# Kernel tuning notes

Hardware: AMD Instinct MI355X
Metric: run time of the kernel (lower is better)

The kernel has to match this reference:

```python
import jax, jax.numpy as jnp
import numpy as np

L, B, C, S = 4, 256, 512, 64   # layers, batch, channels, spatial (8x8 pooled map)
N = 50000                      # training-bank size per layer
K = 20                         # neighbors for LID


def setup_inputs() -> dict:
    key = jax.random.key(0)
    k1, k2 = jax.random.split(key)
    feats = jax.random.normal(k1, (L, B, C, S), dtype=jnp.float32)
    bank = jax.random.normal(k2, (L, N, C), dtype=jnp.float32)
    return {"feats": feats, "bank": bank, "k": K}


def reference(feats, bank, k):
    # per-layer spatial mean pool: f.view(B, C, -1).mean(dim=2)
    q = feats.mean(axis=-1)                                   # [L, B, C]
    # pairwise Euclidean distances query-vs-bank per layer
    q2 = jnp.sum(q * q, axis=-1)                              # [L, B]
    b2 = jnp.sum(bank * bank, axis=-1)                        # [L, N]
    cross = jnp.einsum('lbc,lnc->lbn', q, bank)               # [L, B, N]
    d2 = q2[:, :, None] + b2[:, None, :] - 2.0 * cross
    dist = jnp.sqrt(jnp.maximum(d2, 0.0))                     # [L, B, N]
    # k+1 smallest distances, ascending (sklearn kneighbors), drop nearest
    neg_top, _ = jax.lax.top_k(-dist, k + 1)                  # [L, B, k+1]
    dk = -neg_top[..., 1:]                                    # [L, B, k] ascending
    r_k = dk[..., -1:]                                        # k-th NN distance
    logs = jnp.log(dk / r_k)                                  # [L, B, k]
    lids = -(k / jnp.sum(logs, axis=-1))                      # [L, B]
    return jnp.transpose(lids, (1, 0))                        # [B, L]
```

## Files before the change

### kernel.cpp

```cpp
#include <hip/hip_runtime.h>
#include <hip/hip_bf16.h>

#define L_ 4
#define B_ 256
#define C_ 512
#define N_ 50000
#define K_ 20
#define NLIST 21
#define NCH 128
#define BIGF 3.0e38f
#define BN 64
#define KS 32
#define NKS 16
#define NT_ 7

#define BS0_O 0u
#define BS1_O 4096u
#define B2V_O 8192u
#define SD_O  8448u
#define SMEM_BYTES 45056

typedef __attribute__((ext_vector_type(8))) short short8;
typedef __attribute__((ext_vector_type(4))) float f32x4;

__device__ __forceinline__ unsigned pk2(float lo, float hi) {
    __hip_bfloat162 h = __float22bfloat162_rn(make_float2(lo, hi));
    return *reinterpret_cast<unsigned*>(&h);
}
__device__ __forceinline__ float sq4(float4 v) {
    return v.x*v.x + v.y*v.y + v.z*v.z + v.w*v.w;
}

#define LGKM_BAR() do { asm volatile("s_waitcnt lgkmcnt(0)" ::: "memory"); \
                        __builtin_amdgcn_s_barrier(); } while (0)

__global__ void qmean_kernel(const float* __restrict__ feats,
                             unsigned short* __restrict__ qbf)
{
    int gtid = blockIdx.x * 256 + threadIdx.x;
    int wid  = gtid >> 6;
    int lane = threadIdx.x & 63;
    const float4* src = reinterpret_cast<const float4*>(feats) + (size_t)wid * 64 + lane;
    float4 v = *src;
    float s = v.x + v.y + v.z + v.w;
    s += __shfl_xor(s, 1); s += __shfl_xor(s, 2);
    s += __shfl_xor(s, 4); s += __shfl_xor(s, 8);
    if ((lane & 15) == 0) {
        const int flat = wid * 4 + (lane >> 4);
        const int c    = flat & (C_ - 1);
        const int rowg = flat >> 9;
        const int l    = rowg >> 8;
        const int b    = rowg & (B_ - 1);
        const int kb = c >> 5, rh = (c >> 3) & 3, e = c & 7;
        const int band = b >> 5, m = (b >> 4) & 1, cl = b & 15;
        const size_t idx =
            ((size_t)(((l*16 + kb)*8 + band)*2 + m)*4 + rh)*128 + cl*8 + e;
        __hip_bfloat16 h = __float2bfloat16(s * (1.0f / 64.0f));
        qbf[idx] = *reinterpret_cast<unsigned short*>(&h);
    }
}

__global__ __launch_bounds__(512, 4)
void dist_topk_kernel(const float* __restrict__ bank,
                      const unsigned short* __restrict__ qbf,
                      float* __restrict__ lists)
{
    __shared__ __align__(16) unsigned char smem[SMEM_BYTES];
    float* b2v = reinterpret_cast<float*>(smem + B2V_O);
    float* sd  = reinterpret_cast<float*>(smem + SD_O);
    float* mg  = reinterpret_cast<float*>(smem);

    const int tid = threadIdx.x;
    const int l   = blockIdx.x >> 7;
    const int nc  = blockIdx.x & 127;

    const float* bb = bank + (size_t)l * N_ * C_;
    const int n0   = (nc * 3125) >> 3;
    const int n1   = ((nc + 1) * 3125) >> 3;
    const int n1m1 = n1 - 1;

    const int lane = tid & 63;
    const int wv   = tid >> 6;
    const int c_lo = lane & 15;
    const int r_hi = lane >> 4;

    const unsigned short* qf0 = qbf + (size_t)l * 131072 + wv * 1024 + lane * 8;
    const unsigned short* qf1 = qf0 + 512;

    const int brow   = tid >> 3;
    const int b_srck = ((((tid >> 1) & 3) ^ ((brow >> 1) & 3)) << 3) + ((tid & 1) << 2);
    const unsigned b_dst = (unsigned)tid << 3;

    unsigned offB[4];
#pragma unroll
    for (int n = 0; n < 4; ++n) {
        const int row = n*16 + c_lo;
        offB[n] = (unsigned)(row*64 + ((r_hi ^ ((row >> 1) & 3)) << 4));
    }

    float list[NLIST];
#pragma unroll
    for (int i = 0; i < NLIST; ++i) list[i] = BIGF;

    float4 rr[4];
    short8 qa, qb_;
    float  b2a = 0.f, b2_keep = 0.f;

    {
        const float* ba0 = bb + (size_t)min(n0 + brow, n1m1) * C_ + b_srck;
#pragma unroll
        for (int s4 = 0; s4 < 4; ++s4)
            rr[s4] = *reinterpret_cast<const float4*>(
                reinterpret_cast<const char*>(ba0) + s4 * (KS * 4));
        const float4 v = rr[0];
        b2a = sq4(v);
        uint2 pk_; pk_.x = pk2(v.x, v.y); pk_.y = pk2(v.z, v.w);
        *reinterpret_cast<uint2*>(smem + BS0_O + b_dst) = pk_;
        qa  = *reinterpret_cast<const short8*>(qf0);
        qb_ = *reinterpret_cast<const short8*>(qf1);
        LGKM_BAR();
    }

#pragma unroll 1
    for (int t = 0; t < NT_; ++t) {
        const int nt = n0 + t * BN;
        const float* baddrA = bb + (size_t)min(nt + brow,      n1m1) * C_ + b_srck;
        const float* baddrB = bb + (size_t)min(nt + BN + brow, n1m1) * C_ + b_srck;

        f32x4 acc[2][4];
#pragma unroll
        for (int m = 0; m < 2; ++m)
#pragma unroll
            for (int n = 0; n < 4; ++n) acc[m][n] = (f32x4){0.f, 0.f, 0.f, 0.f};

#pragma unroll
        for (int s = 0; s < NKS; ++s) {
            {
                const float4 v = rr[(s + 1) & 3];
                const float s2 = sq4(v);
                if (s == NKS - 1) { b2_keep = b2a; b2a = s2; } else b2a += s2;
                uint2 pk_; pk_.x = pk2(v.x, v.y); pk_.y = pk2(v.z, v.w);
                *reinterpret_cast<uint2*>(smem + ((s + 1) & 1 ? BS1_O : BS0_O) + b_dst) = pk_;
            }
            {
                const float* ba = (s >= NKS - 4) ? baddrB : baddrA;
                rr[s & 3] = *reinterpret_cast<const float4*>(
                    reinterpret_cast<const char*>(ba) + ((s + 4) & 15) * (KS * 4));
            }
            {
                const unsigned bso = (s & 1) ? BS1_O : BS0_O;
#pragma unroll
                for (int n = 0; n < 4; ++n) {
                    const short8 bn = *reinterpret_cast<const short8*>(smem + bso + offB[n]);
                    acc[0][n] = __builtin_amdgcn_mfma_f32_16x16x32_bf16(qa,  bn, acc[0][n], 0, 0, 0);
                    acc[1][n] = __builtin_amdgcn_mfma_f32_16x16x32_bf16(qb_, bn, acc[1][n], 0, 0, 0);
                }
            }
            {
                const int kb2 = ((s + 1) & 15) * 8192;
                qa  = *reinterpret_cast<const short8*>(qf0 + kb2);
                qb_ = *reinterpret_cast<const short8*>(qf1 + kb2);
            }
            LGKM_BAR();
        }

        {
            float v = b2_keep;
            v += __shfl_xor(v, 1); v += __shfl_xor(v, 2); v += __shfl_xor(v, 4);
            if ((tid & 7) == 0) b2v[brow] = v;
        }
        LGKM_BAR();

#pragma unroll
        for (int ph = 0; ph < 2; ++ph) {
#pragma unroll
            for (int m = 0; m < 2; ++m)
#pragma unroll
                for (int nn = 0; nn < 2; ++nn) {
                    const int n    = 2*ph + nn;
                    const int col  = 16*n + c_lo;
                    const int lcol = 16*nn + c_lo;
                    const float bv = b2v[col];
                    const bool ok  = (nt + col) < n1;
#pragma unroll
                    for (int rg = 0; rg < 4; ++rg) {
                        const int row = wv*32 + m*16 + r_hi*4 + rg;
                        const float v = fmaf(-2.0f, acc[m][n][rg], bv);
                        sd[row*34 + lcol] = ok ? v : BIGF;
                    }
                }
            LGKM_BAR();
            {
                const float* srow = sd + (tid >> 1)*34 + ((tid & 1) << 4);
#pragma unroll
                for (int bt = 0; bt < 4; ++bt) {
                    const float2 u = *reinterpret_cast<const float2*>(srow + (bt << 2));
                    const float2 w = *reinterpret_cast<const float2*>(srow + (bt << 2) + 2);
                    const float m4 = fminf(fminf(u.x, u.y), fminf(w.x, w.y));
                    if (m4 < list[NLIST-1]) {
                        float cand[4] = {u.x, u.y, w.x, w.y};
#pragma unroll
                        for (int c4 = 0; c4 < 4; ++c4) {
                            float v = cand[c4];
                            if (v < list[NLIST-1]) {
#pragma unroll
                                for (int i = 0; i < NLIST; ++i) {
                                    const float lo = fminf(list[i], v);
                                    const float hi = fmaxf(list[i], v);
                                    list[i] = lo; v = hi;
                                }
                            }
                        }
                    }
                }
            }
            LGKM_BAR();
        }
    }

#pragma unroll
    for (int i = 0; i < NLIST; ++i) mg[tid*22 + i] = list[i];
    LGKM_BAR();
    if ((tid & 1) == 0) {
        const int row = tid >> 1;
        float* outp = lists + ((size_t)(l*B_ + row)*NCH + nc)*NLIST;
        const float* g0 = mg + tid*22;
        const float* g1 = mg + (tid + 1)*22;
        int p0 = 0, p1 = 0;
#pragma unroll 1
        for (int i = 0; i < NLIST; ++i) {
            const float h0 = (p0 < NLIST) ? g0[p0] : BIGF;
            const float h1 = (p1 < NLIST) ? g1[p1] : BIGF;
            if (h0 <= h1) { outp[i] = h0; ++p0; }
            else          { outp[i] = h1; ++p1; }
        }
    }
}

__global__ void lid_kernel(const float* __restrict__ lists,
                           const unsigned short* __restrict__ qbf,
                           float* __restrict__ out)
{
    __shared__ float pops[4][NLIST];
    const int lane = threadIdx.x & 63;
    const int w    = threadIdx.x >> 6;
    const int gw   = blockIdx.x * 4 + w;
    const int l    = gw & 3;
    const int b    = gw >> 2;

    const size_t qidx =
        ((size_t)(((l*16 + (lane >> 2))*8 + (b >> 5))*2 + ((b >> 4) & 1))*4 + (lane & 3))*128
        + (size_t)(b & 15)*8;
    short8 qv = *reinterpret_cast<const short8*>(qbf + qidx);
    float q2 = 0.f;
#pragma unroll
    for (int i = 0; i < 8; ++i) {
        unsigned u = ((unsigned)(unsigned short)qv[i]) << 16;
        float f = __uint_as_float(u);
        q2 += f*f;
    }
    q2 += __shfl_xor(q2,1); q2 += __shfl_xor(q2,2); q2 += __shfl_xor(q2,4);
    q2 += __shfl_xor(q2,8); q2 += __shfl_xor(q2,16); q2 += __shfl_xor(q2,32);

    const float* base = lists + (size_t)(l*B_ + b) * NCH * NLIST;
    int p0 = 0, p1 = 0;
#pragma unroll 1
    for (int i = 0; i < NLIST; ++i) {
        const float h0 = (p0 < NLIST) ? base[(size_t)lane*NLIST + p0] : BIGF;
        const float h1 = (p1 < NLIST) ? base[(size_t)(lane+64)*NLIST + p1] : BIGF;
        const float h  = fminf(h0, h1);
        float m = h;
        m = fminf(m, __shfl_xor(m,1));  m = fminf(m, __shfl_xor(m,2));
        m = fminf(m, __shfl_xor(m,4));  m = fminf(m, __shfl_xor(m,8));
        m = fminf(m, __shfl_xor(m,16)); m = fminf(m, __shfl_xor(m,32));
        const unsigned long long ball = __ballot(h == m);
        if (lane == __ffsll(ball) - 1) {
            if (h0 == m) ++p0;
            else         ++p1;
        }
        if (lane == 0) pops[w][i] = fmaxf(q2 + m, 0.f);
    }
    __syncthreads();

    const float r2 = pops[w][NLIST-1];
    float t = 0.f;
    if (lane >= 1 && lane < NLIST) t = 0.5f * logf(pops[w][lane] / r2);
    t += __shfl_xor(t,1); t += __shfl_xor(t,2); t += __shfl_xor(t,4);
    t += __shfl_xor(t,8); t += __shfl_xor(t,16); t += __shfl_xor(t,32);

    if (lane == 0) out[(size_t)b * L_ + l] = -(float)K_ / t;
}

extern "C" void kernel_launch(void* const* d_in, const int* in_sizes, int n_in,
                              void* d_out, int out_size, void* d_ws, size_t ws_size,
                              hipStream_t stream)
{
    (void)in_sizes; (void)n_in; (void)out_size; (void)ws_size;
    const float* feats = (const float*)d_in[0];
    const float* bank  = (const float*)d_in[1];
    unsigned short* qbf = (unsigned short*)d_ws;
    float* lists = (float*)((char*)d_ws + (size_t)L_*B_*C_*2);

    qmean_kernel<<<32768, 256, 0, stream>>>(feats, qbf);
    dist_topk_kernel<<<L_*NCH, 512, 0, stream>>>(bank, qbf, lists);
    lid_kernel<<<256, 256, 0, stream>>>(lists, qbf, (float*)d_out);
}
```

Before: 268.7 us.

## Double the K-slab per LDS stage to halve barriers in the distance GEMM

The bank tile pipeline now stages 64 channels per LDS buffer (two 16x16x32 MFMA k-steps per stage) instead of 32, with wider 16-byte packed bf16 stores, a new XOR swizzle over 8 chunks, and 8 stages per tile instead of 16. This cuts the number of workgroup barriers and LDS round-trips in the main loop and interleaves query-fragment loads between the two MFMA groups. It also drops the trailing barrier after the second selection phase, relying on the next tile's barriers. The cost is doubled LDS buffer size and more live registers, which could lower occupancy.

New measurement: 286.5 us. 6.6% more time.

```diff
diff --git a/kernel.cpp b/kernel.cpp
--- a/kernel.cpp
+++ b/kernel.cpp
@@ -10,15 +10,14 @@
 #define NCH 128
 #define BIGF 3.0e38f
 #define BN 64
-#define KS 32
-#define NKS 16
+#define NW 8
 #define NT_ 7
 
 #define BS0_O 0u
-#define BS1_O 4096u
-#define B2V_O 8192u
-#define SD_O  8448u
-#define SMEM_BYTES 45056
+#define BS1_O 8192u
+#define B2V_O 16384u
+#define SD_O  16640u
+#define SMEM_BYTES 51456
 
 typedef __attribute__((ext_vector_type(8))) short short8;
 typedef __attribute__((ext_vector_type(4))) float f32x4;
@@ -84,40 +83,47 @@
     const int c_lo = lane & 15;
     const int r_hi = lane >> 4;
 
-    const unsigned short* qf0 = qbf + (size_t)l * 131072 + wv * 1024 + lane * 8;
-    const unsigned short* qf1 = qf0 + 512;
+    const unsigned short* qf = qbf + (size_t)l * 131072 + wv * 1024 + lane * 8;
 
     const int brow   = tid >> 3;
-    const int b_srck = ((((tid >> 1) & 3) ^ ((brow >> 1) & 3)) << 3) + ((tid & 1) << 2);
-    const unsigned b_dst = (unsigned)tid << 3;
-
-    unsigned offB[4];
+    const int b_srck = (((tid & 7) ^ (brow & 7)) << 3);
+    const unsigned b_dst = (unsigned)tid << 4;
+
+    unsigned offB[4][2];
 #pragma unroll
     for (int n = 0; n < 4; ++n) {
         const int row = n*16 + c_lo;
-        offB[n] = (unsigned)(row*64 + ((r_hi ^ ((row >> 1) & 3)) << 4));
+#pragma unroll
+        for (int kb = 0; kb < 2; ++kb)
+            offB[n][kb] = (unsigned)(row*128 + (((kb*4 + r_hi) ^ (row & 7)) << 4));
     }
 
     float list[NLIST];
 #pragma unroll
     for (int i = 0; i < NLIST; ++i) list[i] = BIGF;
 
-    float4 rr[4];
-    short8 qa, qb_;
+    float4 ring[4][2];
+    short8 a1m0, a1m1;
+    short8 a2m0, a2m1;
     float  b2a = 0.f, b2_keep = 0.f;
 
     {
         const float* ba0 = bb + (size_t)min(n0 + brow, n1m1) * C_ + b_srck;
 #pragma unroll
-        for (int s4 = 0; s4 < 4; ++s4)
-            rr[s4] = *reinterpret_cast<const float4*>(
-                reinterpret_cast<const char*>(ba0) + s4 * (KS * 4));
-        const float4 v = rr[0];
-        b2a = sq4(v);
-        uint2 pk_; pk_.x = pk2(v.x, v.y); pk_.y = pk2(v.z, v.w);
-        *reinterpret_cast<uint2*>(smem + BS0_O + b_dst) = pk_;
-        qa  = *reinterpret_cast<const short8*>(qf0);
-        qb_ = *reinterpret_cast<const short8*>(qf1);
+        for (int d = 0; d < 4; ++d) {
+            ring[d][0] = *reinterpret_cast<const float4*>(
+                reinterpret_cast<const char*>(ba0) + d * 256);
+            ring[d][1] = *reinterpret_cast<const float4*>(
+                reinterpret_cast<const char*>(ba0) + d * 256 + 16);
+        }
+        a1m0 = *reinterpret_cast<const short8*>(qf);
+        a1m1 = *reinterpret_cast<const short8*>(qf + 512);
+        const float4 v0 = ring[0][0], v1 = ring[0][1];
+        b2a = sq4(v0) + sq4(v1);
+        union { short8 s; unsigned u[4]; } pk;
+        pk.u[0] = pk2(v0.x,v0.y); pk.u[1] = pk2(v0.z,v0.w);
+        pk.u[2] = pk2(v1.x,v1.y); pk.u[3] = pk2(v1.z,v1.w);
+        *reinterpret_cast<short8*>(smem + BS0_O + b_dst) = pk.s;
         LGKM_BAR();
     }
 
@@ -134,32 +140,45 @@
             for (int n = 0; n < 4; ++n) acc[m][n] = (f32x4){0.f, 0.f, 0.f, 0.f};
 
 #pragma unroll
-        for (int s = 0; s < NKS; ++s) {
-            {
-                const float4 v = rr[(s + 1) & 3];
-                const float s2 = sq4(v);
-                if (s == NKS - 1) { b2_keep = b2a; b2a = s2; } else b2a += s2;
-                uint2 pk_; pk_.x = pk2(v.x, v.y); pk_.y = pk2(v.z, v.w);
-                *reinterpret_cast<uint2*>(smem + ((s + 1) & 1 ? BS1_O : BS0_O) + b_dst) = pk_;
-            }
-            {
-                const float* ba = (s >= NKS - 4) ? baddrB : baddrA;
-                rr[s & 3] = *reinterpret_cast<const float4*>(
-                    reinterpret_cast<const char*>(ba) + ((s + 4) & 15) * (KS * 4));
-            }
-            {
-                const unsigned bso = (s & 1) ? BS1_O : BS0_O;
+        for (int w = 0; w < NW; ++w) {
+            {
+                const float4 v0 = ring[(w + 1) & 3][0], v1 = ring[(w + 1) & 3][1];
+                const float s2 = sq4(v0) + sq4(v1);
+                if (w == NW - 1) { b2_keep = b2a; b2a = s2; } else b2a += s2;
+                union { short8 s; unsigned u[4]; } pk;
+                pk.u[0] = pk2(v0.x,v0.y); pk.u[1] = pk2(v0.z,v0.w);
+                pk.u[2] = pk2(v1.x,v1.y); pk.u[3] = pk2(v1.z,v1.w);
+                *reinterpret_cast<short8*>(smem + ((w + 1) & 1 ? BS1_O : BS0_O) + b_dst) = pk.s;
+            }
+            {
+                const float* ba = (w < 4) ? baddrA : baddrB;
+                const int d = (w + 4) & 7;
+                ring[w & 3][0] = *reinterpret_cast<const float4*>(
+                    reinterpret_cast<const char*>(ba) + d * 256);
+                ring[w & 3][1] = *reinterpret_cast<const float4*>(
+                    reinterpret_cast<const char*>(ba) + d * 256 + 16);
+            }
+            a2m0 = *reinterpret_cast<const short8*>(qf + (2*w + 1) * 8192);
+            a2m1 = *reinterpret_cast<const short8*>(qf + (2*w + 1) * 8192 + 512);
+            {
+                const unsigned bso = (w & 1) ? BS1_O : BS0_O;
 #pragma unroll
                 for (int n = 0; n < 4; ++n) {
-                    const short8 bn = *reinterpret_cast<const short8*>(smem + bso + offB[n]);
-                    acc[0][n] = __builtin_amdgcn_mfma_f32_16x16x32_bf16(qa,  bn, acc[0][n], 0, 0, 0);
-                    acc[1][n] = __builtin_amdgcn_mfma_f32_16x16x32_bf16(qb_, bn, acc[1][n], 0, 0, 0);
+                    const short8 bn = *reinterpret_cast<const short8*>(smem + bso + offB[n][0]);
+                    acc[0][n] = __builtin_amdgcn_mfma_f32_16x16x32_bf16(a1m0, bn, acc[0][n], 0, 0, 0);
+                    acc[1][n] = __builtin_amdgcn_mfma_f32_16x16x32_bf16(a1m1, bn, acc[1][n], 0, 0, 0);
                 }
             }
-            {
-                const int kb2 = ((s + 1) & 15) * 8192;
-                qa  = *reinterpret_cast<const short8*>(qf0 + kb2);
-                qb_ = *reinterpret_cast<const short8*>(qf1 + kb2);
+            a1m0 = *reinterpret_cast<const short8*>(qf + (2*((w + 1) & 7)) * 8192);
+            a1m1 = *reinterpret_cast<const short8*>(qf + (2*((w + 1) & 7)) * 8192 + 512);
+            {
+                const unsigned bso = (w & 1) ? BS1_O : BS0_O;
+#pragma unroll
+                for (int n = 0; n < 4; ++n) {
+                    const short8 bn = *reinterpret_cast<const short8*>(smem + bso + offB[n][1]);
+                    acc[0][n] = __builtin_amdgcn_mfma_f32_16x16x32_bf16(a2m0, bn, acc[0][n], 0, 0, 0);
+                    acc[1][n] = __builtin_amdgcn_mfma_f32_16x16x32_bf16(a2m1, bn, acc[1][n], 0, 0, 0);
+                }
             }
             LGKM_BAR();
         }
@@ -195,10 +214,10 @@
 #pragma unroll
                 for (int bt = 0; bt < 4; ++bt) {
                     const float2 u = *reinterpret_cast<const float2*>(srow + (bt << 2));
-                    const float2 w = *reinterpret_cast<const float2*>(srow + (bt << 2) + 2);
-                    const float m4 = fminf(fminf(u.x, u.y), fminf(w.x, w.y));
+                    const float2 w2 = *reinterpret_cast<const float2*>(srow + (bt << 2) + 2);
+                    const float m4 = fminf(fminf(u.x, u.y), fminf(w2.x, w2.y));
                     if (m4 < list[NLIST-1]) {
-                        float cand[4] = {u.x, u.y, w.x, w.y};
+                        float cand[4] = {u.x, u.y, w2.x, w2.y};
 #pragma unroll
                         for (int c4 = 0; c4 < 4; ++c4) {
                             float v = cand[c4];
@@ -214,10 +233,11 @@
                     }
                 }
             }
-            LGKM_BAR();
-        }
-    }
-
+            if (ph == 0) LGKM_BAR();
+        }
+    }
+
+    LGKM_BAR();
 #pragma unroll
     for (int i = 0; i < NLIST; ++i) mg[tid*22 + i] = list[i];
     LGKM_BAR();
```
